# Kernel optimization log

Hardware: AMD Instinct MI355X
Metric: run time of the kernel (lower is better)

The kernel has to match this reference:

```python
import jax, jax.numpy as jnp
import numpy as np

NUM_GROUPS = 6
K = 40
CODEBOOK = 1024
VQ_COMMIT = 0.25


def setup_inputs() -> dict:
    key = jax.random.key(0)
    k1, k2 = jax.random.split(key)
    z = jax.random.normal(k1, (32, 60, 8000), dtype=jnp.float32)
    embeddings = jax.random.normal(k2, (NUM_GROUPS, K, CODEBOOK), dtype=jnp.float32)
    return {"z": z, "embeddings": embeddings}


def reference(z, embeddings):
    # z: (N, 60, T) -> reshape to (N, 240, T//4) as in Group_Quantize.forward
    N, C, T = z.shape
    z2 = z.reshape(N, C * 4, -1)          # (N, 240, Tp)
    Tp = z2.shape[-1]
    # split into groups and move channel last (EMAQuantizer transposes 1,-1)
    x = z2.reshape(N, NUM_GROUPS, K, Tp)
    x = jnp.transpose(x, (1, 0, 3, 2))    # (G, N, Tp, K)
    flat = x.reshape(NUM_GROUPS, N * Tp, K)  # (G, R, K)

    dist = (jnp.sum(flat ** 2, axis=-1, keepdims=True)
            - 2.0 * jnp.einsum('grk,gkc->grc', flat, embeddings)
            + jnp.sum(embeddings ** 2, axis=1)[:, None, :])  # (G, R, C)
    idx = jnp.argmin(dist, axis=-1)       # (G, R)

    # codebook lookup per group (embedding stored as (K, C), code vectors are columns)
    quant = jax.vmap(lambda e, i: jnp.take(e.T, i, axis=0))(embeddings, idx)  # (G, R, K)

    x4 = x                                 # (G, N, Tp, K)
    q4 = quant.reshape(NUM_GROUPS, N, Tp, K)

    # commitment loss per group, per batch element
    diff = VQ_COMMIT * jnp.mean((jax.lax.stop_gradient(q4) - x4) ** 2, axis=(2, 3))  # (G, N)
    vq_loss = jnp.sum(diff, axis=0) / NUM_GROUPS  # (N,)

    # straight-through estimator
    q_ste = x4 + jax.lax.stop_gradient(q4 - x4)   # (G, N, Tp, K)
    q_merge = jnp.transpose(q_ste, (1, 0, 3, 2)).reshape(N, NUM_GROUPS * K, Tp)  # (N, 240, Tp)
    q_merge = q_merge.reshape(N, (NUM_GROUPS * K) // 4, -1)  # (N, 60, T)
    return q_merge, vq_loss
```

## Files before the change

kernel.cpp:

```cpp
#include <hip/hip_runtime.h>
#include <math.h>

#define NG 6
#define KD 40
#define CB 1024
#define NB 32
#define TP 2000
#define RPB 128
#define THREADS 256
#define NBLK 500
#define ZN 480000
#define ZG 80000
#define BAND_D 6e-3f
#define PK_G 98304
#define PK_T 3072
#define CHS 6144
#define NCH 16

typedef __attribute__((ext_vector_type(8))) short bf16x8;
typedef __attribute__((ext_vector_type(16))) float f32x16;

__device__ __forceinline__ unsigned short bf16rne(float v) {
  unsigned u = __float_as_uint(v);
  return (unsigned short)((u + 0x7FFFu + ((u >> 16) & 1u)) >> 16);
}
__device__ __forceinline__ float bf16val(unsigned short h) {
  return __uint_as_float(((unsigned)h) << 16);
}
__device__ __forceinline__ void bf16split(float v, unsigned short& h, unsigned short& l) {
  h = bf16rne(v);
  l = bf16rne(v - bf16val(h));
}
__device__ __forceinline__ bf16x8 ldfrag16(const unsigned short* p) {
  union { uint4 q; bf16x8 v; } u;
  u.q = *(const uint4*)p;
  return u.v;
}
__device__ __forceinline__ void gload_lds16(const void* g, void* l) {
  __builtin_amdgcn_global_load_lds(
      (const __attribute__((address_space(1))) unsigned int*)g,
      (__attribute__((address_space(3))) unsigned int*)l, 16, 0, 0);
}

__global__ void prep_kernel(const float* __restrict__ emb, float* __restrict__ et,
                            float* __restrict__ e2, unsigned short* __restrict__ epack) {
  int c = blockIdx.x * blockDim.x + threadIdx.x;
  int g = blockIdx.y;
  if (c >= CB) return;
  const float* eg = emb + (size_t)g * KD * CB;
  float ev[KD];
  float* o = et + ((size_t)g * CB + c) * KD;
  float s = 0.f;
#pragma unroll
  for (int k = 0; k < KD; ++k) {
    float v = eg[k * CB + c];
    ev[k] = v;
    o[k] = v;
    s = __fadd_rn(s, __fmul_rn(v, v));
  }
  e2[g * CB + c] = s;

  float sv = 0.5f * s;
  unsigned short p0 = bf16rne(sv);
  float v1 = sv - bf16val(p0);
  unsigned short p1 = bf16rne(v1);
  unsigned short p2 = bf16rne(v1 - bf16val(p1));

  int tile = c >> 5, j32 = c & 31;
  unsigned short* tb = epack + (size_t)g * PK_G + (size_t)tile * PK_T;
#pragma unroll
  for (int s2 = 0; s2 < 3; ++s2)
#pragma unroll
    for (int gg = 0; gg < 2; ++gg) {
      union { uint4 q; unsigned short sh[8]; } uh, ul;
#pragma unroll
      for (int j = 0; j < 8; ++j) {
        int k = s2 * 16 + gg * 8 + j;
        if (k < KD) {
          bf16split(ev[k], uh.sh[j], ul.sh[j]);
        } else {
          uh.sh[j] = (k == 40) ? p0 : (k == 41) ? p1 : (k == 42) ? p2 : (unsigned short)0;
          ul.sh[j] = 0;
        }
      }
      unsigned short* ph = tb + ((size_t)(s2 * 2 + gg) * 32 + j32) * 8;
      *(uint4*)ph = uh.q;
      *(uint4*)(ph + 1536) = ul.q;
    }
}

__device__ __forceinline__ float npd_calc(const float* __restrict__ x,
                                          const float* __restrict__ ef,
                                          float e2c, float x2np) {
  float dot = 0.f;
#pragma unroll
  for (int k = 0; k < KD; ++k) dot = __fadd_rn(dot, __fmul_rn(x[k], ef[k]));
  return __fadd_rn(__fsub_rn(x2np, __fadd_rn(dot, dot)), e2c);
}

__global__ __launch_bounds__(THREADS, 3) void vq_kernel(
    const float* __restrict__ z, const float* __restrict__ et,
    const float* __restrict__ e2, const unsigned short* __restrict__ epack,
    float* __restrict__ out, float* __restrict__ partials) {
  const int g = blockIdx.y;
  const int bb = blockIdx.x;
  const int tid = threadIdx.x;
  const int lane = tid & 63;
  const int gg = lane >> 5;
  const int j32 = lane & 31;
  const int wid = tid >> 6;
  const int rowloc = wid * 32 + j32;
  const int rid = bb * RPB + rowloc;
  const int n = rid / TP;
  const int tt = rid - n * TP;

  const float* etg = et + (size_t)g * CB * KD;
  const float* e2g = e2 + g * CB;
  const unsigned short* egrp = epack + (size_t)g * PK_G;

  __shared__ __align__(16) unsigned short sbuf[3][CHS];
  __shared__ float r0s[THREADS], r1s[THREADS];

#define STAGE(B, CH) { \
    const unsigned short* gsrc = egrp + (size_t)(CH) * CHS + wid * 512 + lane * 8; \
    unsigned short* lb = &sbuf[B][wid * 512]; \
    gload_lds16(gsrc, lb); \
    gload_lds16(gsrc + 2048, lb + 2048); \
    gload_lds16(gsrc + 4096, lb + 4096); }
  STAGE(0, 0)
  STAGE(1, 1)

  const float* zp = z + (size_t)n * ZN + (size_t)g * ZG + tt;
  float x[KD];
#pragma unroll
  for (int k = 0; k < KD; ++k) x[k] = zp[(size_t)k * TP];
  float x2np;
  {
    float r[8];
#pragma unroll
    for (int j = 0; j < 8; ++j) r[j] = __fmul_rn(x[j], x[j]);
#pragma unroll
    for (int i = 8; i < KD; i += 8)
#pragma unroll
      for (int j = 0; j < 8; ++j)
        r[j] = __fadd_rn(r[j], __fmul_rn(x[i + j], x[i + j]));
    x2np = __fadd_rn(__fadd_rn(__fadd_rn(r[0], r[1]), __fadd_rn(r[2], r[3])),
                     __fadd_rn(__fadd_rn(r[4], r[5]), __fadd_rn(r[6], r[7])));
  }

  bf16x8 xh[3], xl[3];
#define PACK8(DH, DL, B0) { \
    union { unsigned short s[8]; bf16x8 v; } uh, ul; \
    _Pragma("unroll") \
    for (int j = 0; j < 8; ++j) { \
      unsigned short h, l; bf16split(-x[(B0) + j], h, l); \
      uh.s[j] = h; ul.s[j] = l; } \
    DH = uh.v; DL = ul.v; }
  if (gg == 0) {
    PACK8(xh[0], xl[0], 0)
    PACK8(xh[1], xl[1], 16)
    PACK8(xh[2], xl[2], 32)
  } else {
    PACK8(xh[0], xl[0], 8)
    PACK8(xh[1], xl[1], 24)
    union { unsigned short s[8]; bf16x8 v; } uh;
#pragma unroll
    for (int j = 0; j < 8; ++j) uh.s[j] = (j < 3) ? (unsigned short)0x3F80 : (unsigned short)0;
    xh[2] = uh.v;
    union { unsigned short s[8]; bf16x8 v; } uz;
#pragma unroll
    for (int j = 0; j < 8; ++j) uz.s[j] = 0;
    xl[2] = uz.v;
  }
#undef PACK8

  f32x16 zacc;
#pragma unroll
  for (int i = 0; i < 16; ++i) zacc[i] = 0.f;

  float d1 = INFINITY, d2x = INFINITY;
  int grp1 = 0;

#define TRACKG(AV, TILE) { \
    int cb = (TILE) * 32 + 4 * gg; \
    float q0 = fminf(fminf(fminf(AV[0], AV[1]), AV[2]), AV[3]); \
    float q1 = fminf(fminf(fminf(AV[4], AV[5]), AV[6]), AV[7]); \
    float q2 = fminf(fminf(fminf(AV[8], AV[9]), AV[10]), AV[11]); \
    float q3 = fminf(fminf(fminf(AV[12], AV[13]), AV[14]), AV[15]); \
    d2x = fminf(d2x, fmaxf(d1, q0)); grp1 = (q0 < d1) ? (cb + 0) : grp1; d1 = fminf(d1, q0); \
    d2x = fminf(d2x, fmaxf(d1, q1)); grp1 = (q1 < d1) ? (cb + 8) : grp1; d1 = fminf(d1, q1); \
    d2x = fminf(d2x, fmaxf(d1, q2)); grp1 = (q2 < d1) ? (cb + 16) : grp1; d1 = fminf(d1, q2); \
    d2x = fminf(d2x, fmaxf(d1, q3)); grp1 = (q3 < d1) ? (cb + 24) : grp1; d1 = fminf(d1, q3); }

#define MFMA9(TB, AOUT) { \
    bf16x8 eh0 = ldfrag16(TB); \
    bf16x8 eh1 = ldfrag16((TB) + 512); \
    bf16x8 eh2 = ldfrag16((TB) + 1024); \
    bf16x8 el0 = ldfrag16((TB) + 1536); \
    bf16x8 el1 = ldfrag16((TB) + 2048); \
    bf16x8 el2 = ldfrag16((TB) + 2560); \
    AOUT = __builtin_amdgcn_mfma_f32_32x32x16_bf16(eh0, xh[0], zacc, 0, 0, 0); \
    AOUT = __builtin_amdgcn_mfma_f32_32x32x16_bf16(eh0, xl[0], AOUT, 0, 0, 0); \
    AOUT = __builtin_amdgcn_mfma_f32_32x32x16_bf16(el0, xh[0], AOUT, 0, 0, 0); \
    AOUT = __builtin_amdgcn_mfma_f32_32x32x16_bf16(eh1, xh[1], AOUT, 0, 0, 0); \
    AOUT = __builtin_amdgcn_mfma_f32_32x32x16_bf16(eh1, xl[1], AOUT, 0, 0, 0); \
    AOUT = __builtin_amdgcn_mfma_f32_32x32x16_bf16(el1, xh[1], AOUT, 0, 0, 0); \
    AOUT = __builtin_amdgcn_mfma_f32_32x32x16_bf16(eh2, xh[2], AOUT, 0, 0, 0); \
    AOUT = __builtin_amdgcn_mfma_f32_32x32x16_bf16(eh2, xl[2], AOUT, 0, 0, 0); \
    AOUT = __builtin_amdgcn_mfma_f32_32x32x16_bf16(el2, xh[2], AOUT, 0, 0, 0); }

  int cur = 0, stg = 2;
#pragma unroll 1
  for (int ch = 0; ch < NCH; ++ch) {
    if (ch < NCH - 1) {
      asm volatile("s_waitcnt vmcnt(3)" ::: "memory");
    } else {
      asm volatile("s_waitcnt vmcnt(0)" ::: "memory");
    }
    __builtin_amdgcn_s_barrier();
    if (ch + 2 < NCH) STAGE(stg, ch + 2)
    {
      f32x16 a0, a1;
      MFMA9(&sbuf[cur][lane * 8], a0)
      MFMA9(&sbuf[cur][PK_T + lane * 8], a1)
      TRACKG(a0, ch * 2)
      TRACKG(a1, ch * 2 + 1)
    }
    cur = (cur == 2) ? 0 : cur + 1;
    stg = (stg == 2) ? 0 : stg + 1;
  }

  float bd = INFINITY;
  int bi = CB;
#pragma unroll
  for (int j = 0; j < 4; ++j) {
    int c = grp1 + j;
    float d = npd_calc(x, etg + (size_t)c * KD, e2g[c], x2np);
    if (d < bd) { bd = d; bi = c; }
  }
  float dd2x = fmaf(2.f, d2x, x2np);

  {
    float od = __shfl_xor(bd, 32);
    int oi = __shfl_xor(bi, 32);
    float odd2x = __shfl_xor(dd2x, 32);
    if (od < bd || (od == bd && oi < bi)) { bd = od; bi = oi; }
    dd2x = fminf(dd2x, odd2x);
  }
  bool flag = dd2x < bd + BAND_D;

  if (__any(flag)) {
    float rd1 = INFINITY, rd2 = INFINITY, rd3 = INFINITY;
    int ri1 = 0, ri2 = 0, ri3 = 0;
#define INS3(V, C) { \
      bool u1 = (V) < rd1, u2 = (V) < rd2, u3 = (V) < rd3; \
      rd3 = u2 ? rd2 : (u3 ? (V) : rd3); ri3 = u2 ? ri2 : (u3 ? (C) : ri3); \
      rd2 = u1 ? rd1 : (u2 ? (V) : rd2); ri2 = u1 ? ri1 : (u2 ? (C) : ri2); \
      rd1 = u1 ? (V) : rd1;              ri1 = u1 ? (C) : ri1; }
#pragma unroll 1
    for (int tile = 0; tile < 32; ++tile) {
      const unsigned short* tb = egrp + (size_t)tile * PK_T + lane * 8;
      f32x16 a;
      MFMA9(tb, a)
      {
        float gm0 = fminf(fminf(a[0], a[1]), fminf(a[2], a[3]));
        float gm1 = fminf(fminf(a[4], a[5]), fminf(a[6], a[7]));
        float gm2 = fminf(fminf(a[8], a[9]), fminf(a[10], a[11]));
        float gm3 = fminf(fminf(a[12], a[13]), fminf(a[14], a[15]));
        float tmin = fminf(fminf(gm0, gm1), fminf(gm2, gm3));
        if (tmin < rd3) {
          int cb = tile * 32 + 4 * gg;
          if (gm0 < rd3) { INS3(a[0], cb + 0) INS3(a[1], cb + 1) INS3(a[2], cb + 2) INS3(a[3], cb + 3) }
          if (gm1 < rd3) { INS3(a[4], cb + 8) INS3(a[5], cb + 9) INS3(a[6], cb + 10) INS3(a[7], cb + 11) }
          if (gm2 < rd3) { INS3(a[8], cb + 16) INS3(a[9], cb + 17) INS3(a[10], cb + 18) INS3(a[11], cb + 19) }
          if (gm3 < rd3) { INS3(a[12], cb + 24) INS3(a[13], cb + 25) INS3(a[14], cb + 26) INS3(a[15], cb + 27) }
        }
      }
    }
    float dd1 = fmaf(2.f, rd1, x2np);
    float dd2 = fmaf(2.f, rd2, x2np);
    float dd3 = fmaf(2.f, rd3, x2np);
    bd = dd1; bi = ri1;
    bool exact = false;
    {
      bool need2 = dd2 < dd1 + BAND_D;
      bool need3 = dd3 < dd1 + BAND_D;
      if (need2 || need3) {
        int cA = ri1;
        int cB = need2 ? ri2 : 0x7fffffff;
        int cC = need3 ? ri3 : 0x7fffffff;
        int t;
        if (cA > cB) { t = cA; cA = cB; cB = t; }
        if (cB > cC) { t = cB; cB = cC; cC = t; }
        if (cA > cB) { t = cA; cA = cB; cB = t; }
        bd = INFINITY; bi = CB;
        if (cA < CB) { float d = npd_calc(x, etg + (size_t)cA * KD, e2g[cA], x2np); if (d < bd) { bd = d; bi = cA; } }
        if (cB < CB) { float d = npd_calc(x, etg + (size_t)cB * KD, e2g[cB], x2np); if (d < bd) { bd = d; bi = cB; } }
        if (cC < CB) { float d = npd_calc(x, etg + (size_t)cC * KD, e2g[cC], x2np); if (d < bd) { bd = d; bi = cC; } }
        exact = true;
      }
    }
    {
      float od = __shfl_xor(bd, 32);
      bool race = fabsf(bd - od) < BAND_D;
      if (race && !exact) bd = npd_calc(x, etg + (size_t)bi * KD, e2g[bi], x2np);
      float od2 = __shfl_xor(bd, 32);
      int oi = __shfl_xor(bi, 32);
      if (od2 < bd || (od2 == bd && oi < bi)) { bd = od2; bi = oi; }
    }
  }

  const float4* eb4 = (const float4*)(etg + (size_t)bi * KD);
  float* op = out + (size_t)n * ZN + (size_t)g * ZG + tt;
  float ls = 0.f;
  if (gg == 0) {
#pragma unroll
    for (int p = 0; p < 5; ++p) {
      float4 v = eb4[p];
      int k = 4 * p;
      float e0 = __fsub_rn(v.x, x[k + 0]); ls = fmaf(e0, e0, ls); op[(size_t)(k + 0) * TP] = __fadd_rn(x[k + 0], e0);
      float e1 = __fsub_rn(v.y, x[k + 1]); ls = fmaf(e1, e1, ls); op[(size_t)(k + 1) * TP] = __fadd_rn(x[k + 1], e1);
      float e2v = __fsub_rn(v.z, x[k + 2]); ls = fmaf(e2v, e2v, ls); op[(size_t)(k + 2) * TP] = __fadd_rn(x[k + 2], e2v);
      float e3 = __fsub_rn(v.w, x[k + 3]); ls = fmaf(e3, e3, ls); op[(size_t)(k + 3) * TP] = __fadd_rn(x[k + 3], e3);
    }
  } else {
#pragma unroll
    for (int p = 5; p < 10; ++p) {
      float4 v = eb4[p];
      int k = 4 * p;
      float e0 = __fsub_rn(v.x, x[k + 0]); ls = fmaf(e0, e0, ls); op[(size_t)(k + 0) * TP] = __fadd_rn(x[k + 0], e0);
      float e1 = __fsub_rn(v.y, x[k + 1]); ls = fmaf(e1, e1, ls); op[(size_t)(k + 1) * TP] = __fadd_rn(x[k + 1], e1);
      float e2v = __fsub_rn(v.z, x[k + 2]); ls = fmaf(e2v, e2v, ls); op[(size_t)(k + 2) * TP] = __fadd_rn(x[k + 2], e2v);
      float e3 = __fsub_rn(v.w, x[k + 3]); ls = fmaf(e3, e3, ls); op[(size_t)(k + 3) * TP] = __fadd_rn(x[k + 3], e3);
    }
  }

  const int n_lo = (bb * RPB) / TP;
  r0s[tid] = (n == n_lo) ? ls : 0.f;
  r1s[tid] = (n == n_lo) ? 0.f : ls;
  __syncthreads();
  for (int s = THREADS / 2; s > 0; s >>= 1) {
    if (tid < s) {
      r0s[tid] += r0s[tid + s];
      r1s[tid] += r1s[tid + s];
    }
    __syncthreads();
  }
  if (tid == 0) {
    partials[((size_t)g * NBLK + bb) * 2 + 0] = r0s[0];
    partials[((size_t)g * NBLK + bb) * 2 + 1] = r1s[0];
  }
}

__global__ void loss_kernel(const float* __restrict__ partials,
                            float* __restrict__ vq) {
  int n = threadIdx.x;
  if (n >= NB) return;
  float acc = 0.f;
  for (int g = 0; g < NG; ++g) {
    float s = 0.f;
    int b0 = (n * TP) / RPB;
    int b1 = ((n + 1) * TP - 1) / RPB;
    for (int b = b0; b <= b1; ++b) {
      int n_lo = (b * RPB) / TP;
      s += partials[((size_t)g * NBLK + b) * 2 + ((n == n_lo) ? 0 : 1)];
    }
    acc += 0.25f * (s / 80000.0f);
  }
  vq[n] = acc / 6.0f;
}

extern "C" void kernel_launch(void* const* d_in, const int* in_sizes, int n_in,
                              void* d_out, int out_size, void* d_ws, size_t ws_size,
                              hipStream_t stream) {
  const float* z = (const float*)d_in[0];
  const float* emb = (const float*)d_in[1];
  float* out = (float*)d_out;

  float* et = (float*)d_ws;
  float* e2 = et + (size_t)NG * CB * KD;
  float* partials = e2 + (size_t)NG * CB;
  unsigned short* epack = (unsigned short*)((char*)d_ws + 1031680);

  prep_kernel<<<dim3(CB / 256, NG), 256, 0, stream>>>(emb, et, e2, epack);
  vq_kernel<<<dim3(NBLK, NG), THREADS, 0, stream>>>(z, et, e2, epack, out, partials);
  loss_kernel<<<1, 64, 0, stream>>>(partials, out + (size_t)NB * 60 * 8000);
}
```

Measured before the change: 205.9 us.

## Load codebook fragments directly into registers instead of staging through LDS

Removes the triple-buffered LDS staging of packed bf16 codebook tiles with global_load_lds and per-chunk barriers. Each wave now loads its MFMA operand fragments straight from global memory into registers, double-buffered across two tiles and prefetched one iteration ahead. This drops the workgroup barriers and LDS traffic, but every wave now fetches the codebook separately through L1/L2 rather than sharing one staged copy, and it uses more registers.

```diff
diff --git a/kernel.cpp b/kernel.cpp
--- a/kernel.cpp
+++ b/kernel.cpp
@@ -14,8 +14,6 @@
 #define BAND_D 6e-3f
 #define PK_G 98304
 #define PK_T 3072
-#define CHS 6144
-#define NCH 16
 
 typedef __attribute__((ext_vector_type(8))) short bf16x8;
 typedef __attribute__((ext_vector_type(16))) float f32x16;
@@ -30,16 +28,16 @@
 __device__ __forceinline__ void bf16split(float v, unsigned short& h, unsigned short& l) {
   h = bf16rne(v);
   l = bf16rne(v - bf16val(h));
+}
+__device__ __forceinline__ bf16x8 asbf(uint4 q) {
+  union { uint4 q; bf16x8 v; } u;
+  u.q = q;
+  return u.v;
 }
 __device__ __forceinline__ bf16x8 ldfrag16(const unsigned short* p) {
   union { uint4 q; bf16x8 v; } u;
   u.q = *(const uint4*)p;
   return u.v;
-}
-__device__ __forceinline__ void gload_lds16(const void* g, void* l) {
-  __builtin_amdgcn_global_load_lds(
-      (const __attribute__((address_space(1))) unsigned int*)g,
-      (__attribute__((address_space(3))) unsigned int*)l, 16, 0, 0);
 }
 
 __global__ void prep_kernel(const float* __restrict__ emb, float* __restrict__ et,
@@ -117,18 +115,17 @@
   const float* etg = et + (size_t)g * CB * KD;
   const float* e2g = e2 + g * CB;
   const unsigned short* egrp = epack + (size_t)g * PK_G;
-
-  __shared__ __align__(16) unsigned short sbuf[3][CHS];
+  const unsigned short* lanep = egrp + lane * 8;
+
   __shared__ float r0s[THREADS], r1s[THREADS];
 
-#define STAGE(B, CH) { \
-    const unsigned short* gsrc = egrp + (size_t)(CH) * CHS + wid * 512 + lane * 8; \
-    unsigned short* lb = &sbuf[B][wid * 512]; \
-    gload_lds16(gsrc, lb); \
-    gload_lds16(gsrc + 2048, lb + 2048); \
-    gload_lds16(gsrc + 4096, lb + 4096); }
-  STAGE(0, 0)
-  STAGE(1, 1)
+  uint4 fA[6], fB[6];
+#define LDT(F, T) { \
+    const uint4* p4 = (const uint4*)(lanep + (size_t)(T) * PK_T); \
+    F[0] = p4[0];   F[1] = p4[64];  F[2] = p4[128]; \
+    F[3] = p4[192]; F[4] = p4[256]; F[5] = p4[320]; }
+  LDT(fA, 0)
+  LDT(fB, 1)
 
   const float* zp = z + (size_t)n * ZN + (size_t)g * ZG + tt;
   float x[KD];
@@ -192,6 +189,17 @@
     d2x = fminf(d2x, fmaxf(d1, q2)); grp1 = (q2 < d1) ? (cb + 16) : grp1; d1 = fminf(d1, q2); \
     d2x = fminf(d2x, fmaxf(d1, q3)); grp1 = (q3 < d1) ? (cb + 24) : grp1; d1 = fminf(d1, q3); }
 
+#define MFMA9R(F, AOUT) { \
+    AOUT = __builtin_amdgcn_mfma_f32_32x32x16_bf16(asbf(F[0]), xh[0], zacc, 0, 0, 0); \
+    AOUT = __builtin_amdgcn_mfma_f32_32x32x16_bf16(asbf(F[0]), xl[0], AOUT, 0, 0, 0); \
+    AOUT = __builtin_amdgcn_mfma_f32_32x32x16_bf16(asbf(F[3]), xh[0], AOUT, 0, 0, 0); \
+    AOUT = __builtin_amdgcn_mfma_f32_32x32x16_bf16(asbf(F[1]), xh[1], AOUT, 0, 0, 0); \
+    AOUT = __builtin_amdgcn_mfma_f32_32x32x16_bf16(asbf(F[1]), xl[1], AOUT, 0, 0, 0); \
+    AOUT = __builtin_amdgcn_mfma_f32_32x32x16_bf16(asbf(F[4]), xh[1], AOUT, 0, 0, 0); \
+    AOUT = __builtin_amdgcn_mfma_f32_32x32x16_bf16(asbf(F[2]), xh[2], AOUT, 0, 0, 0); \
+    AOUT = __builtin_amdgcn_mfma_f32_32x32x16_bf16(asbf(F[2]), xl[2], AOUT, 0, 0, 0); \
+    AOUT = __builtin_amdgcn_mfma_f32_32x32x16_bf16(asbf(F[5]), xh[2], AOUT, 0, 0, 0); }
+
 #define MFMA9(TB, AOUT) { \
     bf16x8 eh0 = ldfrag16(TB); \
     bf16x8 eh1 = ldfrag16((TB) + 512); \
@@ -209,25 +217,15 @@
     AOUT = __builtin_amdgcn_mfma_f32_32x32x16_bf16(eh2, xl[2], AOUT, 0, 0, 0); \
     AOUT = __builtin_amdgcn_mfma_f32_32x32x16_bf16(el2, xh[2], AOUT, 0, 0, 0); }
 
-  int cur = 0, stg = 2;
 #pragma unroll 1
-  for (int ch = 0; ch < NCH; ++ch) {
-    if (ch < NCH - 1) {
-      asm volatile("s_waitcnt vmcnt(3)" ::: "memory");
-    } else {
-      asm volatile("s_waitcnt vmcnt(0)" ::: "memory");
-    }
-    __builtin_amdgcn_s_barrier();
-    if (ch + 2 < NCH) STAGE(stg, ch + 2)
-    {
-      f32x16 a0, a1;
-      MFMA9(&sbuf[cur][lane * 8], a0)
-      MFMA9(&sbuf[cur][PK_T + lane * 8], a1)
-      TRACKG(a0, ch * 2)
-      TRACKG(a1, ch * 2 + 1)
-    }
-    cur = (cur == 2) ? 0 : cur + 1;
-    stg = (stg == 2) ? 0 : stg + 1;
+  for (int t = 0; t < 32; t += 2) {
+    f32x16 a0, a1;
+    MFMA9R(fA, a0)
+    LDT(fA, (t + 2) & 31)
+    TRACKG(a0, t)
+    MFMA9R(fB, a1)
+    LDT(fB, (t + 3) & 31)
+    TRACKG(a1, t + 1)
   }
 
   float bd = INFINITY;
```

New measurement: 239.0 us. 1.16x slower.
